# Optimization experiments

Measured on AMD Instinct MI355X. Metric: run time of the kernel, lower is better.

The kernel has to match this reference:

```python
import jax, jax.numpy as jnp
import numpy as np

N_NODES = 50000
N_EDGES = 1600000
IN_FEATS = 256
OUT_FEATS = 64


def setup_inputs() -> dict:
    key = jax.random.key(0)
    k_x, k_w, k_b, k_s, k_d = jax.random.split(key, 5)
    x = jax.random.normal(k_x, (N_NODES, IN_FEATS), dtype=jnp.float32)
    # nn.Linear(in_feats, out_feats): weight [out, in], bias [out]
    W = jax.random.normal(k_w, (OUT_FEATS, IN_FEATS), dtype=jnp.float32) / np.sqrt(IN_FEATS)
    b = jax.random.normal(k_b, (OUT_FEATS,), dtype=jnp.float32) * 0.01
    edge_src = jax.random.randint(k_s, (N_EDGES,), 0, N_NODES, dtype=jnp.int32)
    edge_dst = jax.random.randint(k_d, (N_EDGES,), 0, N_NODES, dtype=jnp.int32)
    return {"x": x, "W": W, "b": b, "edge_src": edge_src, "edge_dst": edge_dst}


def reference(x, W, b, edge_src, edge_dst):
    # h = dropout(relu(Linear(x)))  -- dropout p=0 (eval) => identity
    h = jax.nn.relu(x @ W.T + b)                     # [N, out_feats]
    # update_all: message = h[src], reduce = mean over incoming edges per dst
    msg = h[edge_src]                                # [E, out_feats] gather
    summed = jax.ops.segment_sum(msg, edge_dst, num_segments=N_NODES)  # [N, out]
    deg = jax.ops.segment_sum(jnp.ones((edge_src.shape[0],), dtype=h.dtype),
                              edge_dst, num_segments=N_NODES)          # [N]
    deg = jnp.maximum(deg, 1.0)
    return summed / deg[:, None]
```

## Files before the change

### kernel.cpp

```cpp
#include <hip/hip_runtime.h>
#include <hip/hip_bf16.h>

#define K_IN 256
#define O_OUT 64
#define NBINS 1024
#define NPB 49
#define CAP 1824
#define PART_CHUNK 4096

typedef __attribute__((ext_vector_type(8))) short short8;
typedef __attribute__((ext_vector_type(4))) float f32x4;
typedef __attribute__((ext_vector_type(2))) unsigned u32x2;

#define GLOAD2(dst, base, voff)                                          \
  asm volatile("global_load_dwordx2 %0, %1, %2"                          \
               : "=v"(dst) : "v"(voff), "s"(base))
__device__ inline void vmwait0() {
  asm volatile("s_waitcnt vmcnt(0)" ::: "memory");
  __builtin_amdgcn_sched_barrier(0);
}

__device__ inline unsigned short bf16bits(float a) {
  __hip_bfloat16 t = __float2bfloat16(a);
  return *(unsigned short*)&t;
}

__device__ inline short8 cvt8(float4 f0, float4 f1) {
  short8 r;
  r[0] = (short)bf16bits(f0.x); r[1] = (short)bf16bits(f0.y);
  r[2] = (short)bf16bits(f0.z); r[3] = (short)bf16bits(f0.w);
  r[4] = (short)bf16bits(f1.x); r[5] = (short)bf16bits(f1.y);
  r[6] = (short)bf16bits(f1.z); r[7] = (short)bf16bits(f1.w);
  return r;
}

__global__ __launch_bounds__(256) void k_prep(const float* __restrict__ W,
                                              unsigned short* __restrict__ Wb,
                                              int* __restrict__ cursor) {
  int i = blockIdx.x * 256 + threadIdx.x;
  Wb[i] = bf16bits(W[i]);
  if (i < NBINS) cursor[i] = 0;
}

struct GemmSmem {
  unsigned short wsb[64 * 256];
  unsigned short xs[64 * 256];
};
struct PartSmem {
  int cnt[NBINS];
  int scanb[NBINS];
  int gbase[NBINS];
  int wsum[4];
  unsigned ord[PART_CHUNK];
};
union FusedSmem {
  GemmSmem g;
  PartSmem p;
};

__device__ void gemm_body(GemmSmem& sm, int gid, const float* __restrict__ x,
                          const unsigned short* __restrict__ Wb,
                          const float* __restrict__ bias,
                          __hip_bfloat16* __restrict__ h, int N) {
  const int tid = threadIdx.x;
  const int lane = tid & 63;
  const int wv = tid >> 6;
  const int n0 = gid * 64;

  {
    const uint4* wsrc = (const uint4*)Wb;
#pragma unroll
    for (int r = 0; r < 8; ++r) {
      uint4 w = wsrc[r * 256 + tid];
      int flat = r * 256 + tid;
      int row = flat >> 5;
      int c16 = flat & 31;
      unsigned byte = (unsigned)(row * 512 + c16 * 16);
      byte ^= (unsigned)((row & 7) << 4);
      *(uint4*)((char*)sm.wsb + byte) = w;
    }
  }

  {
#pragma unroll
    for (int r = 0; r < 8; ++r) {
      int c = r * 256 + tid;
      int row = c >> 5;
      int c16 = c & 31;
      int node = n0 + row;
      if (node > N - 1) node = N - 1;
      const float4* ps = (const float4*)(x + (size_t)node * K_IN + c16 * 8);
      float4 f0 = ps[0];
      float4 f1 = ps[1];
      unsigned byte = (unsigned)(row * 512 + c16 * 16);
      byte ^= (unsigned)((row & 7) << 4);
      *(short8*)((char*)sm.xs + byte) = cvt8(f0, f1);
    }
  }
  __syncthreads();

  const int brow0 = lane & 15;
  const unsigned kb = (unsigned)((lane >> 4) * 16);
  const unsigned bswz = (unsigned)((brow0 & 7) << 4);
  const int arow = wv * 16 + (lane & 15);
  const unsigned aswz = (unsigned)((arow & 7) << 4);
  const unsigned abase = (unsigned)(arow * 512) + kb;

  f32x4 acc[4] = {{0.f, 0.f, 0.f, 0.f}, {0.f, 0.f, 0.f, 0.f},
                  {0.f, 0.f, 0.f, 0.f}, {0.f, 0.f, 0.f, 0.f}};
#pragma unroll
  for (int k8 = 0; k8 < 8; ++k8) {
    unsigned ab = (abase + (unsigned)(k8 * 64)) ^ aswz;
    short8 a = *(const short8*)((const char*)sm.xs + ab);
#pragma unroll
    for (int nt = 0; nt < 4; ++nt) {
      unsigned byte = (unsigned)((brow0 + nt * 16) * 512 + k8 * 64) + kb;
      byte ^= bswz;
      short8 bfr = *(const short8*)((const char*)sm.wsb + byte);
      acc[nt] = __builtin_amdgcn_mfma_f32_16x16x32_bf16(a, bfr, acc[nt], 0, 0, 0);
    }
  }

  const int col = lane & 15;
  const int rbase = (lane >> 4) * 4;
#pragma unroll
  for (int nt = 0; nt < 4; ++nt) {
    float bv = bias[nt * 16 + col];
#pragma unroll
    for (int j = 0; j < 4; ++j) {
      int node = n0 + wv * 16 + rbase + j;
      if (node < N) {
        float v = fmaxf(acc[nt][j] + bv, 0.f);
        h[(size_t)node * O_OUT + nt * 16 + col] = __float2bfloat16(v);
      }
    }
  }
}

__device__ void part_body(PartSmem& sm, int pid, const int* __restrict__ esrc,
                          const int* __restrict__ edst, int* __restrict__ cursor,
                          unsigned* __restrict__ bucket, int E) {
  const int tid = threadIdx.x;
  const int lane = tid & 63;
  const int wid = tid >> 6;
  const int base = pid * PART_CHUNK;

#pragma unroll
  for (int r = 0; r < 4; ++r) sm.cnt[r * 256 + tid] = 0;

  int4 s4[4], d4[4];
#pragma unroll
  for (int r = 0; r < 4; ++r) {
    int e0 = base + r * 1024 + tid * 4;
    if (e0 + 3 < E) {
      s4[r] = *(const int4*)(esrc + e0);
      d4[r] = *(const int4*)(edst + e0);
    } else {
      s4[r] = make_int4(0, 0, 0, 0);
      d4[r] = make_int4(0, 0, 0, 0);
      int* sp = (int*)&s4[r];
      int* dp = (int*)&d4[r];
      for (int j = 0; j < 4; ++j)
        if (e0 + j < E) { sp[j] = esrc[e0 + j]; dp[j] = edst[e0 + j]; }
    }
  }
  __syncthreads();

  unsigned pk[16];
  int rk[16];
#pragma unroll
  for (int r = 0; r < 4; ++r) {
    const int* sp = (const int*)&s4[r];
    const int* dp = (const int*)&d4[r];
#pragma unroll
    for (int j = 0; j < 4; ++j) {
      int k = r * 4 + j;
      int e = base + r * 1024 + tid * 4 + j;
      if (e < E) {
        int d = dp[j];
        int bb = (int)__umulhi((unsigned)d, 87652394u);
        int dl = d - bb * NPB;
        pk[k] = ((unsigned)sp[j] & 0xFFFFu) | ((unsigned)dl << 16) |
                ((unsigned)bb << 22);
        rk[k] = atomicAdd(&sm.cnt[bb], 1);
      } else {
        rk[k] = -1;
      }
    }
  }
  __syncthreads();

  int c0 = sm.cnt[4 * tid];
  int c1 = sm.cnt[4 * tid + 1];
  int c2 = sm.cnt[4 * tid + 2];
  int c3 = sm.cnt[4 * tid + 3];
  int s = c0 + c1 + c2 + c3;
  int incl = s;
#pragma unroll
  for (int off = 1; off < 64; off <<= 1) {
    int t = __shfl_up(incl, off);
    if (lane >= off) incl += t;
  }
  if (lane == 63) sm.wsum[wid] = incl;
  __syncthreads();
  int wpre = 0;
  for (int w = 0; w < wid; ++w) wpre += sm.wsum[w];
  int excl = wpre + incl - s;
  sm.scanb[4 * tid] = excl;
  sm.scanb[4 * tid + 1] = excl + c0;
  sm.scanb[4 * tid + 2] = excl + c0 + c1;
  sm.scanb[4 * tid + 3] = excl + c0 + c1 + c2;
  sm.gbase[4 * tid] = (c0 > 0) ? atomicAdd(&cursor[4 * tid], c0) : 0;
  sm.gbase[4 * tid + 1] = (c1 > 0) ? atomicAdd(&cursor[4 * tid + 1], c1) : 0;
  sm.gbase[4 * tid + 2] = (c2 > 0) ? atomicAdd(&cursor[4 * tid + 2], c2) : 0;
  sm.gbase[4 * tid + 3] = (c3 > 0) ? atomicAdd(&cursor[4 * tid + 3], c3) : 0;
  __syncthreads();

#pragma unroll
  for (int k = 0; k < 16; ++k) {
    if (rk[k] >= 0) {
      int bb = (int)(pk[k] >> 22);
      sm.ord[sm.scanb[bb] + rk[k]] = pk[k];
    }
  }
  __syncthreads();

  int nv = E - base;
  if (nv > PART_CHUNK) nv = PART_CHUNK;
  for (int p = tid; p < nv; p += 256) {
    unsigned v = sm.ord[p];
    int bb = v >> 22;
    int slot = sm.gbase[bb] + (p - sm.scanb[bb]);
    if (slot < CAP) bucket[(size_t)bb * CAP + slot] = v;
  }
}

__global__ __launch_bounds__(256, 2) void k_fused(const float* __restrict__ x,
                                                  const unsigned short* __restrict__ Wb,
                                                  const float* __restrict__ bias,
                                                  __hip_bfloat16* __restrict__ h,
                                                  const int* __restrict__ esrc,
                                                  const int* __restrict__ edst,
                                                  int* __restrict__ cursor,
                                                  unsigned* __restrict__ bucket,
                                                  int N, int E) {
  __shared__ FusedSmem sm;
  const int npart = (E + PART_CHUNK - 1) / PART_CHUNK;
  const int b = blockIdx.x;
  if (b % 3 == 1 && b / 3 < npart) {
    part_body(sm.p, b / 3, esrc, edst, cursor, bucket, E);
  } else {
    int skipped = (b + 2) / 3;
    if (skipped > npart) skipped = npart;
    gemm_body(sm.g, b - skipped, x, Wb, bias, h, N);
  }
}

__global__ __launch_bounds__(256, 4) void k_sortagg(const unsigned* __restrict__ bucket,
                                                    const int* __restrict__ cursor,
                                                    const unsigned* __restrict__ h32,
                                                    float* __restrict__ out, int N) {
  __shared__ int hist[NPB];
  __shared__ int offs[NPB];
  __shared__ unsigned short sbuf[CAP + 64];

  const int tid = threadIdx.x;
  const int lane = tid & 63;
  const int wid = tid >> 6;
  const int bin = blockIdx.x;

  if (tid < NPB) hist[tid] = 0;
  __syncthreads();

  int cnt = cursor[bin];
  if (cnt > CAP) cnt = CAP;
  const unsigned* bb = bucket + (size_t)bin * CAP;

  unsigned pk2[2][4];
  int rk2[2][4];
#pragma unroll
  for (int g = 0; g < 2; ++g) {
    int i0 = (g * 256 + tid) * 4;
    uint4 v;
    if (i0 + 3 < cnt) {
      v = *(const uint4*)(bb + i0);
    } else {
      v = make_uint4(0, 0, 0, 0);
      unsigned* vp = (unsigned*)&v;
      for (int j = 0; j < 4; ++j)
        if (i0 + j < cnt) vp[j] = bb[i0 + j];
    }
    const unsigned* vp = (const unsigned*)&v;
#pragma unroll
    for (int j = 0; j < 4; ++j) {
      if (i0 + j < cnt) {
        pk2[g][j] = vp[j];
        rk2[g][j] = atomicAdd(&hist[(vp[j] >> 16) & 63], 1);
      } else {
        rk2[g][j] = -1;
      }
    }
  }
  __syncthreads();

  if (tid < 64) {
    int hval = (tid < NPB) ? hist[tid] : 0;
    int incl = hval;
#pragma unroll
    for (int off = 1; off < 64; off <<= 1) {
      int t = __shfl_up(incl, off);
      if (lane >= off) incl += t;
    }
    if (tid < NPB) offs[tid] = incl - hval;
  }
  __syncthreads();

#pragma unroll
  for (int g = 0; g < 2; ++g)
#pragma unroll
    for (int j = 0; j < 4; ++j)
      if (rk2[g][j] >= 0)
        sbuf[offs[(pk2[g][j] >> 16) & 63] + rk2[g][j]] =
            (unsigned short)(pk2[g][j] & 0xFFFFu);
  __syncthreads();

  const int q = lane >> 4;
  const int hl = lane & 15;
  const unsigned hlb = (unsigned)hl * 8u;

  for (int nl = wid; nl < NPB; nl += 8) {
    const int nlb = nl + 4;
    const bool hasb = (nlb < NPB);
    const int ca = hist[nl];
    const int cb = hasb ? hist[nlb] : 0;
    const unsigned short* bsa = sbuf + offs[nl];
    const unsigned short* bsb = sbuf + (hasb ? offs[nlb] : 0);

    unsigned voa[12], vob[12];
#pragma unroll
    for (int k = 0; k < 12; ++k) {
      int e = k * 4 + q;
      unsigned pa = (e < ca) ? (unsigned)bsa[e] : 0u;
      unsigned pb = (e < cb) ? (unsigned)bsb[e] : 0u;
      voa[k] = pa * 128u + hlb;
      vob[k] = pb * 128u + hlb;
    }
    u32x2 ua[12], ub[12];
#pragma unroll
    for (int k = 0; k < 12; ++k) { GLOAD2(ua[k], h32, voa[k]); }
#pragma unroll
    for (int k = 0; k < 12; ++k) { GLOAD2(ub[k], h32, vob[k]); }
    vmwait0();

    float a0 = 0.f, a1 = 0.f, a2 = 0.f, a3 = 0.f;
    float b0 = 0.f, b1 = 0.f, b2 = 0.f, b3 = 0.f;
#pragma unroll
    for (int k = 0; k < 12; ++k) {
      float wk = (k * 4 + q < ca) ? 1.f : 0.f;
      a0 = fmaf(wk, __uint_as_float(ua[k][0] << 16), a0);
      a1 = fmaf(wk, __uint_as_float(ua[k][0] & 0xFFFF0000u), a1);
      a2 = fmaf(wk, __uint_as_float(ua[k][1] << 16), a2);
      a3 = fmaf(wk, __uint_as_float(ua[k][1] & 0xFFFF0000u), a3);
    }
#pragma unroll
    for (int k = 0; k < 12; ++k) {
      float wk = (k * 4 + q < cb) ? 1.f : 0.f;
      b0 = fmaf(wk, __uint_as_float(ub[k][0] << 16), b0);
      b1 = fmaf(wk, __uint_as_float(ub[k][0] & 0xFFFF0000u), b1);
      b2 = fmaf(wk, __uint_as_float(ub[k][1] << 16), b2);
      b3 = fmaf(wk, __uint_as_float(ub[k][1] & 0xFFFF0000u), b3);
    }

    const uint2* __restrict__ h2 = (const uint2*)h32;
    for (int e0 = 48; e0 < ca; e0 += 4) {
      int e = e0 + q;
      float wk = (e < ca) ? 1.f : 0.f;
      int p = (e < ca) ? (int)bsa[e] : 0;
      uint2 u = h2[(size_t)p * 16 + hl];
      a0 = fmaf(wk, __uint_as_float(u.x << 16), a0);
      a1 = fmaf(wk, __uint_as_float(u.x & 0xFFFF0000u), a1);
      a2 = fmaf(wk, __uint_as_float(u.y << 16), a2);
      a3 = fmaf(wk, __uint_as_float(u.y & 0xFFFF0000u), a3);
    }
    for (int e0 = 48; e0 < cb; e0 += 4) {
      int e = e0 + q;
      float wk = (e < cb) ? 1.f : 0.f;
      int p = (e < cb) ? (int)bsb[e] : 0;
      uint2 u = h2[(size_t)p * 16 + hl];
      b0 = fmaf(wk, __uint_as_float(u.x << 16), b0);
      b1 = fmaf(wk, __uint_as_float(u.x & 0xFFFF0000u), b1);
      b2 = fmaf(wk, __uint_as_float(u.y << 16), b2);
      b3 = fmaf(wk, __uint_as_float(u.y & 0xFFFF0000u), b3);
    }

    a0 += __shfl_xor(a0, 16); a1 += __shfl_xor(a1, 16);
    a2 += __shfl_xor(a2, 16); a3 += __shfl_xor(a3, 16);
    b0 += __shfl_xor(b0, 16); b1 += __shfl_xor(b1, 16);
    b2 += __shfl_xor(b2, 16); b3 += __shfl_xor(b3, 16);
    a0 += __shfl_xor(a0, 32); a1 += __shfl_xor(a1, 32);
    a2 += __shfl_xor(a2, 32); a3 += __shfl_xor(a3, 32);
    b0 += __shfl_xor(b0, 32); b1 += __shfl_xor(b1, 32);
    b2 += __shfl_xor(b2, 32); b3 += __shfl_xor(b3, 32);

    if (lane < 16) {
      int na = bin * NPB + nl;
      if (na < N) {
        float inv = 1.f / fmaxf((float)ca, 1.f);
        float4 r;
        r.x = a0 * inv; r.y = a1 * inv; r.z = a2 * inv; r.w = a3 * inv;
        *(float4*)(out + (size_t)na * O_OUT + hl * 4) = r;
      }
      int nb = bin * NPB + nlb;
      if (hasb && nb < N) {
        float inv = 1.f / fmaxf((float)cb, 1.f);
        float4 r;
        r.x = b0 * inv; r.y = b1 * inv; r.z = b2 * inv; r.w = b3 * inv;
        *(float4*)(out + (size_t)nb * O_OUT + hl * 4) = r;
      }
    }
  }
}

extern "C" void kernel_launch(void* const* d_in, const int* in_sizes, int n_in,
                              void* d_out, int out_size, void* d_ws, size_t ws_size,
                              hipStream_t stream) {
  const float* x = (const float*)d_in[0];
  const float* W = (const float*)d_in[1];
  const float* b = (const float*)d_in[2];
  const int* esrc = (const int*)d_in[3];
  const int* edst = (const int*)d_in[4];
  float* out = (float*)d_out;

  const int N = in_sizes[0] / K_IN;
  const int E = in_sizes[3];

  char* ws = (char*)d_ws;
  unsigned short* Wb = (unsigned short*)ws;
  __hip_bfloat16* h = (__hip_bfloat16*)(ws + 32768);
  size_t off = 32768 + (size_t)N * O_OUT * sizeof(__hip_bfloat16);
  int* cursor = (int*)(ws + off);
  off += NBINS * sizeof(int);
  unsigned* bucket = (unsigned*)(ws + off);

  const int ngemm = (N + 63) / 64;
  const int npart = (E + PART_CHUNK - 1) / PART_CHUNK;

  k_prep<<<(K_IN * O_OUT) / 256, 256, 0, stream>>>(W, Wb, cursor);
  k_fused<<<ngemm + npart, 256, 0, stream>>>(x, Wb, b, h, esrc, edst, cursor,
                                             bucket, N, E);
  k_sortagg<<<NBINS, 256, 0, stream>>>(bucket, cursor, (const unsigned*)h, out, N);
}
```

Measured before the change: 165.2 us.

## Replace atomic global bucketing with per-chunk sorted segments and scan tables

Partition blocks now write their locally bin-sorted chunk and a per-chunk bin offset table instead of reserving global bucket slots with atomics. Each aggregation block then gathers its bin's segments from all chunks into shared memory. This removes the prep kernel, the cursor atomics and the zeroing. The GEMM also converts W to bf16 in place, loads x fragments directly from global into registers instead of staging them in LDS, and halves LDS use so occupancy can rise to 4 blocks. The cost is that the aggregation kernel scans ~391 scan-table entries per bin and does serial, scattered small-segment copies.

```diff
diff --git a/kernel.cpp b/kernel.cpp
--- a/kernel.cpp
+++ b/kernel.cpp
@@ -7,6 +7,7 @@
 #define NPB 49
 #define CAP 1824
 #define PART_CHUNK 4096
+#define SCAN_STRIDE 1026
 
 typedef __attribute__((ext_vector_type(8))) short short8;
 typedef __attribute__((ext_vector_type(4))) float f32x4;
@@ -34,22 +35,12 @@
   return r;
 }
 
-__global__ __launch_bounds__(256) void k_prep(const float* __restrict__ W,
-                                              unsigned short* __restrict__ Wb,
-                                              int* __restrict__ cursor) {
-  int i = blockIdx.x * 256 + threadIdx.x;
-  Wb[i] = bf16bits(W[i]);
-  if (i < NBINS) cursor[i] = 0;
-}
-
 struct GemmSmem {
   unsigned short wsb[64 * 256];
-  unsigned short xs[64 * 256];
 };
 struct PartSmem {
   int cnt[NBINS];
   int scanb[NBINS];
-  int gbase[NBINS];
   int wsum[4];
   unsigned ord[PART_CHUNK];
 };
@@ -59,7 +50,7 @@
 };
 
 __device__ void gemm_body(GemmSmem& sm, int gid, const float* __restrict__ x,
-                          const unsigned short* __restrict__ Wb,
+                          const float* __restrict__ W,
                           const float* __restrict__ bias,
                           __hip_bfloat16* __restrict__ h, int N) {
   const int tid = threadIdx.x;
@@ -68,50 +59,36 @@
   const int n0 = gid * 64;
 
   {
-    const uint4* wsrc = (const uint4*)Wb;
 #pragma unroll
     for (int r = 0; r < 8; ++r) {
-      uint4 w = wsrc[r * 256 + tid];
-      int flat = r * 256 + tid;
-      int row = flat >> 5;
-      int c16 = flat & 31;
+      int c = r * 256 + tid;
+      const float4* ps = (const float4*)(W + c * 8);
+      float4 f0 = ps[0];
+      float4 f1 = ps[1];
+      int row = c >> 5;
+      int c16 = c & 31;
       unsigned byte = (unsigned)(row * 512 + c16 * 16);
       byte ^= (unsigned)((row & 7) << 4);
-      *(uint4*)((char*)sm.wsb + byte) = w;
-    }
-  }
-
-  {
-#pragma unroll
-    for (int r = 0; r < 8; ++r) {
-      int c = r * 256 + tid;
-      int row = c >> 5;
-      int c16 = c & 31;
-      int node = n0 + row;
-      if (node > N - 1) node = N - 1;
-      const float4* ps = (const float4*)(x + (size_t)node * K_IN + c16 * 8);
-      float4 f0 = ps[0];
-      float4 f1 = ps[1];
-      unsigned byte = (unsigned)(row * 512 + c16 * 16);
-      byte ^= (unsigned)((row & 7) << 4);
-      *(short8*)((char*)sm.xs + byte) = cvt8(f0, f1);
-    }
-  }
-  __syncthreads();
+      *(short8*)((char*)sm.wsb + byte) = cvt8(f0, f1);
+    }
+  }
+  __syncthreads();
+
+  int anode = n0 + wv * 16 + (lane & 15);
+  if (anode > N - 1) anode = N - 1;
+  const float* aptr = x + (size_t)anode * K_IN + (lane >> 4) * 8;
 
   const int brow0 = lane & 15;
   const unsigned kb = (unsigned)((lane >> 4) * 16);
   const unsigned bswz = (unsigned)((brow0 & 7) << 4);
-  const int arow = wv * 16 + (lane & 15);
-  const unsigned aswz = (unsigned)((arow & 7) << 4);
-  const unsigned abase = (unsigned)(arow * 512) + kb;
 
   f32x4 acc[4] = {{0.f, 0.f, 0.f, 0.f}, {0.f, 0.f, 0.f, 0.f},
                   {0.f, 0.f, 0.f, 0.f}, {0.f, 0.f, 0.f, 0.f}};
 #pragma unroll
   for (int k8 = 0; k8 < 8; ++k8) {
-    unsigned ab = (abase + (unsigned)(k8 * 64)) ^ aswz;
-    short8 a = *(const short8*)((const char*)sm.xs + ab);
+    float4 f0 = *(const float4*)(aptr + k8 * 32);
+    float4 f1 = *(const float4*)(aptr + k8 * 32 + 4);
+    short8 a = cvt8(f0, f1);
 #pragma unroll
     for (int nt = 0; nt < 4; ++nt) {
       unsigned byte = (unsigned)((brow0 + nt * 16) * 512 + k8 * 64) + kb;
@@ -138,8 +115,9 @@
 }
 
 __device__ void part_body(PartSmem& sm, int pid, const int* __restrict__ esrc,
-                          const int* __restrict__ edst, int* __restrict__ cursor,
-                          unsigned* __restrict__ bucket, int E) {
+                          const int* __restrict__ edst,
+                          unsigned* __restrict__ bucket_det,
+                          unsigned short* __restrict__ scan_tab, int E) {
   const int tid = threadIdx.x;
   const int lane = tid & 63;
   const int wid = tid >> 6;
@@ -210,10 +188,6 @@
   sm.scanb[4 * tid + 1] = excl + c0;
   sm.scanb[4 * tid + 2] = excl + c0 + c1;
   sm.scanb[4 * tid + 3] = excl + c0 + c1 + c2;
-  sm.gbase[4 * tid] = (c0 > 0) ? atomicAdd(&cursor[4 * tid], c0) : 0;
-  sm.gbase[4 * tid + 1] = (c1 > 0) ? atomicAdd(&cursor[4 * tid + 1], c1) : 0;
-  sm.gbase[4 * tid + 2] = (c2 > 0) ? atomicAdd(&cursor[4 * tid + 2], c2) : 0;
-  sm.gbase[4 * tid + 3] = (c3 > 0) ? atomicAdd(&cursor[4 * tid + 3], c3) : 0;
   __syncthreads();
 
 #pragma unroll
@@ -227,39 +201,42 @@
 
   int nv = E - base;
   if (nv > PART_CHUNK) nv = PART_CHUNK;
-  for (int p = tid; p < nv; p += 256) {
-    unsigned v = sm.ord[p];
-    int bb = v >> 22;
-    int slot = sm.gbase[bb] + (p - sm.scanb[bb]);
-    if (slot < CAP) bucket[(size_t)bb * CAP + slot] = v;
-  }
-}
-
-__global__ __launch_bounds__(256, 2) void k_fused(const float* __restrict__ x,
-                                                  const unsigned short* __restrict__ Wb,
+
+  unsigned* dstp = bucket_det + (size_t)pid * PART_CHUNK;
+  for (int p = tid; p < nv; p += 256) dstp[p] = sm.ord[p];
+  unsigned short* st = scan_tab + (size_t)pid * SCAN_STRIDE;
+  for (int i = tid; i < NBINS; i += 256) st[i] = (unsigned short)sm.scanb[i];
+  if (tid == 0) st[NBINS] = (unsigned short)nv;
+}
+
+__global__ __launch_bounds__(256, 4) void k_fused(const float* __restrict__ x,
+                                                  const float* __restrict__ W,
                                                   const float* __restrict__ bias,
                                                   __hip_bfloat16* __restrict__ h,
                                                   const int* __restrict__ esrc,
                                                   const int* __restrict__ edst,
-                                                  int* __restrict__ cursor,
-                                                  unsigned* __restrict__ bucket,
+                                                  unsigned* __restrict__ bucket_det,
+                                                  unsigned short* __restrict__ scan_tab,
                                                   int N, int E) {
   __shared__ FusedSmem sm;
   const int npart = (E + PART_CHUNK - 1) / PART_CHUNK;
   const int b = blockIdx.x;
   if (b % 3 == 1 && b / 3 < npart) {
-    part_body(sm.p, b / 3, esrc, edst, cursor, bucket, E);
+    part_body(sm.p, b / 3, esrc, edst, bucket_det, scan_tab, E);
   } else {
     int skipped = (b + 2) / 3;
     if (skipped > npart) skipped = npart;
-    gemm_body(sm.g, b - skipped, x, Wb, bias, h, N);
-  }
-}
-
-__global__ __launch_bounds__(256, 4) void k_sortagg(const unsigned* __restrict__ bucket,
-                                                    const int* __restrict__ cursor,
+    gemm_body(sm.g, b - skipped, x, W, bias, h, N);
+  }
+}
+
+__global__ __launch_bounds__(256, 4) void k_sortagg(const unsigned* __restrict__ bucket_det,
+                                                    const unsigned short* __restrict__ scan_tab,
                                                     const unsigned* __restrict__ h32,
-                                                    float* __restrict__ out, int N) {
+                                                    float* __restrict__ out,
+                                                    int N, int npart) {
+  __shared__ unsigned ord32[CAP];
+  __shared__ int segbase;
   __shared__ int hist[NPB];
   __shared__ int offs[NPB];
   __shared__ unsigned short sbuf[CAP + 64];
@@ -269,33 +246,50 @@
   const int wid = tid >> 6;
   const int bin = blockIdx.x;
 
+  if (tid == 0) segbase = 0;
   if (tid < NPB) hist[tid] = 0;
   __syncthreads();
 
-  int cnt = cursor[bin];
+#pragma unroll
+  for (int r = 0; r < 2; ++r) {
+    int p = r * 256 + tid;
+    int cnt_p = 0, s = 0;
+    if (p < npart) {
+      const unsigned short* st = scan_tab + (size_t)p * SCAN_STRIDE;
+      s = st[bin];
+      int e = st[bin + 1];
+      cnt_p = e - s;
+    }
+    int incl = cnt_p;
+#pragma unroll
+    for (int off = 1; off < 64; off <<= 1) {
+      int t = __shfl_up(incl, off);
+      if (lane >= off) incl += t;
+    }
+    int base_w = 0;
+    if (lane == 63) base_w = atomicAdd(&segbase, incl);
+    base_w = __shfl(base_w, 63);
+    int myofs = base_w + incl - cnt_p;
+    const unsigned* srcp = bucket_det + (size_t)p * PART_CHUNK + s;
+    for (int j = 0; j < cnt_p; ++j)
+      if (myofs + j < CAP) ord32[myofs + j] = srcp[j];
+  }
+  __syncthreads();
+
+  int cnt = segbase;
   if (cnt > CAP) cnt = CAP;
-  const unsigned* bb = bucket + (size_t)bin * CAP;
 
   unsigned pk2[2][4];
   int rk2[2][4];
 #pragma unroll
   for (int g = 0; g < 2; ++g) {
-    int i0 = (g * 256 + tid) * 4;
-    uint4 v;
-    if (i0 + 3 < cnt) {
-      v = *(const uint4*)(bb + i0);
-    } else {
-      v = make_uint4(0, 0, 0, 0);
-      unsigned* vp = (unsigned*)&v;
-      for (int j = 0; j < 4; ++j)
-        if (i0 + j < cnt) vp[j] = bb[i0 + j];
-    }
-    const unsigned* vp = (const unsigned*)&v;
 #pragma unroll
     for (int j = 0; j < 4; ++j) {
-      if (i0 + j < cnt) {
-        pk2[g][j] = vp[j];
-        rk2[g][j] = atomicAdd(&hist[(vp[j] >> 16) & 63], 1);
+      int i = (g * 256 + tid) * 4 + j;
+      if (i < cnt) {
+        unsigned w = ord32[i];
+        pk2[g][j] = w;
+        rk2[g][j] = atomicAdd(&hist[(w >> 16) & 63], 1);
       } else {
         rk2[g][j] = -1;
       }
@@ -433,20 +427,18 @@
 
   const int N = in_sizes[0] / K_IN;
   const int E = in_sizes[3];
+  const int npart = (E + PART_CHUNK - 1) / PART_CHUNK;
+  const int ngemm = (N + 63) / 64;
 
   char* ws = (char*)d_ws;
-  unsigned short* Wb = (unsigned short*)ws;
-  __hip_bfloat16* h = (__hip_bfloat16*)(ws + 32768);
-  size_t off = 32768 + (size_t)N * O_OUT * sizeof(__hip_bfloat16);
-  int* cursor = (int*)(ws + off);
-  off += NBINS * sizeof(int);
-  unsigned* bucket = (unsigned*)(ws + off);
-
-  const int ngemm = (N + 63) / 64;
-  const int npart = (E + PART_CHUNK - 1) / PART_CHUNK;
-
-  k_prep<<<(K_IN * O_OUT) / 256, 256, 0, stream>>>(W, Wb, cursor);
-  k_fused<<<ngemm + npart, 256, 0, stream>>>(x, Wb, b, h, esrc, edst, cursor,
-                                             bucket, N, E);
-  k_sortagg<<<NBINS, 256, 0, stream>>>(bucket, cursor, (const unsigned*)h, out, N);
-}
+  __hip_bfloat16* h = (__hip_bfloat16*)ws;
+  size_t off = (size_t)N * O_OUT * sizeof(__hip_bfloat16);
+  unsigned* bucket_det = (unsigned*)(ws + off);
+  off += (size_t)npart * PART_CHUNK * sizeof(unsigned);
+  unsigned short* scan_tab = (unsigned short*)(ws + off);
+
+  k_fused<<<ngemm + npart, 256, 0, stream>>>(x, W, b, h, esrc, edst,
+                                             bucket_det, scan_tab, N, E);
+  k_sortagg<<<NBINS, 256, 0, stream>>>(bucket_det, scan_tab, (const unsigned*)h,
+                                       out, N, npart);
+}
```

After: 151.0 us. 8.6% less time.
